# Kernel tuning notes

Measured on AMD Instinct MI355X. Metric: run time of the kernel, lower is better.

## Reference

```python
import jax, jax.numpy as jnp
import numpy as np

RADIUS = 0.1
NSAMPLE = 32
STRIDE = 4
EPS = 1e-5


def fps(p, M):
    # Furthest point sampling. p: [B, N, 3] -> idx [B, M] int32. First point is index 0.
    B, N, _ = p.shape

    def body(carry, _):
        dmin, last = carry
        lp = jnp.take_along_axis(p, last[:, None, None], axis=1)  # [B,1,3]
        d = jnp.sum((p - lp) ** 2, axis=-1)                       # [B,N]
        dmin = jnp.minimum(dmin, d)
        nxt = jnp.argmax(dmin, axis=-1).astype(jnp.int32)
        return (dmin, nxt), nxt

    first = jnp.zeros((B,), jnp.int32)
    dmin0 = jnp.full((B, N), jnp.inf, p.dtype)
    _, rest = jax.lax.scan(body, (dmin0, first), None, length=M - 1)
    return jnp.concatenate([first[None, :], rest], axis=0).T  # [B,M]


def ball_query(new_p, p, radius, K):
    # For each query, first K support indices with dist < radius (CUDA ballquery semantics:
    # pad with first found index; 0 if none). new_p [B,M,3], p [B,N,3] -> [B,M,K] int32.
    N = p.shape[1]
    d2 = (jnp.sum(new_p ** 2, -1)[:, :, None] + jnp.sum(p ** 2, -1)[:, None, :]
          - 2.0 * jnp.einsum('bmd,bnd->bmn', new_p, p))  # [B,M,N]
    scores = jnp.where(d2 < radius * radius,
                       jnp.arange(N, dtype=jnp.int32)[None, None, :], N)
    neg_vals, _ = jax.lax.top_k(-scores, K)  # K smallest scores, ascending
    idx = -neg_vals
    first = jnp.where(idx[..., :1] >= N, 0, idx[..., :1])
    return jnp.where(idx >= N, first, idx)


def bn(x, g, b):
    # BatchNorm (training-mode batch stats) over all dims except channel dim 1.
    axes = tuple(i for i in range(x.ndim) if i != 1)
    m = jnp.mean(x, axes, keepdims=True)
    v = jnp.var(x, axes, keepdims=True)
    shape = (1, -1) + (1,) * (x.ndim - 2)
    return g.reshape(shape) * (x - m) * jax.lax.rsqrt(v + EPS) + b.reshape(shape)


def setup_inputs() -> dict:
    key = jax.random.key(0)
    ks = jax.random.split(key, 6)
    B, N, C = 4, 8192, 64
    return {
        'p': jax.random.uniform(ks[0], (B, N, 3), jnp.float32),
        'f': jax.random.normal(ks[1], (B, C, N), jnp.float32),
        'w1': jax.random.normal(ks[2], (64, 3 + C), jnp.float32) * 0.05,
        'g1': jnp.ones((64,), jnp.float32),
        'b1': jnp.zeros((64,), jnp.float32),
        'w2': jax.random.normal(ks[3], (128, 64), jnp.float32) * 0.05,
        'g2': jnp.ones((128,), jnp.float32),
        'b2': jnp.zeros((128,), jnp.float32),
        'w_skip': jax.random.normal(ks[4], (128, C), jnp.float32) * 0.05,
        'b_skip': jnp.zeros((128,), jnp.float32),
    }


def reference(p, f, w1, g1, b1, w2, g2, b2, w_skip, b_skip):
    B, N, _ = p.shape
    C = f.shape[1]
    M = N // STRIDE
    idx = fps(p, M)                                                # [B,M]
    new_p = jnp.take_along_axis(p, idx[:, :, None], axis=1)        # [B,M,3]
    # residual branch: gather sampled features, 1x1 conv1d skip
    fi = jnp.take_along_axis(f, jnp.broadcast_to(idx[:, None, :], (B, C, M)), axis=2)
    identity = jnp.einsum('oc,bcm->bom', w_skip, fi) + b_skip[None, :, None]
    # ball-query grouping
    nidx = ball_query(new_p, p, RADIUS, NSAMPLE)                   # [B,M,K]
    flat = nidx.reshape(B, 1, M * NSAMPLE)
    pj = jnp.take_along_axis(p.transpose(0, 2, 1),
                             jnp.broadcast_to(flat, (B, 3, M * NSAMPLE)),
                             axis=2).reshape(B, 3, M, NSAMPLE)
    dp = pj - new_p.transpose(0, 2, 1)[:, :, :, None]              # [B,3,M,K]
    fj = jnp.take_along_axis(f, jnp.broadcast_to(flat, (B, C, M * NSAMPLE)),
                             axis=2).reshape(B, C, M, NSAMPLE)
    x = jnp.concatenate([dp, fj], axis=1)                          # [B,3+C,M,K]
    # conv-bn-relu, conv-bn (last block no act because use_res)
    x = jax.nn.relu(bn(jnp.einsum('oc,bcmk->bomk', w1, x), g1, b1))
    x = bn(jnp.einsum('oc,bcmk->bomk', w2, x), g2, b2)
    fout = jnp.max(x, axis=-1)                                     # [B,128,M]
    fout = jax.nn.relu(fout + identity)
    return new_p, fout, idx
```

## Files before the change

### kernel.cpp

```cpp
#include <hip/hip_runtime.h>
#include <math.h>

#define BB 4
#define NP 8192
#define CF 64
#define MQ 2048
#define KS 32

#define WS_FT     0u
#define WS_NIDX   2097152u
#define WS_IDXI   2359296u
#define WS_ST1    2367488u
#define WS_ST2    2375680u
#define WS_SC1    2392064u
#define WS_SC2    2392192u
#define WS_MAXY2  2392448u
#define WS_W1P    3441024u

typedef float v2f __attribute__((ext_vector_type(2)));

__global__ __launch_bounds__(256) void transpose_f_kernel(
    const float* __restrict__ f, float* __restrict__ ft) {
  __shared__ float tile[64][65];
  int b = blockIdx.y;
  int n0 = blockIdx.x * 64;
  int cc = threadIdx.x >> 6;
  int nn = threadIdx.x & 63;
  #pragma unroll
  for (int r = 0; r < 16; ++r) {
    int c = cc * 16 + r;
    tile[c][nn] = f[((size_t)b * 64 + c) * NP + n0 + nn];
  }
  __syncthreads();
  #pragma unroll
  for (int r = 0; r < 16; ++r) {
    int nl = cc * 16 + r;
    ft[((size_t)b * NP + n0 + nl) * 64 + nn] = tile[nn][nl];
  }
}

__global__ void prep_w1_kernel(const float* __restrict__ w1, float* __restrict__ w1p) {
  int i = blockIdx.x * 256 + threadIdx.x;
  if (i < 64 * 68) {
    int o = i / 68, c = i % 68;
    w1p[i] = (c < 67) ? w1[o * 67 + c] : 0.0f;
  }
}

#define FPS_T 256
#define PPT 32

template <int CTRL>
__device__ __forceinline__ unsigned long long dpp_max_step(unsigned long long k) {
  int lo = (int)(unsigned)k;
  int hi = (int)(unsigned)(k >> 32);
  int slo = __builtin_amdgcn_update_dpp(0, lo, CTRL, 0xF, 0xF, true);
  int shi = __builtin_amdgcn_update_dpp(0, hi, CTRL, 0xF, 0xF, true);
  unsigned long long s =
      ((unsigned long long)(unsigned)shi << 32) | (unsigned long long)(unsigned)slo;
  return s > k ? s : k;
}

__global__ __launch_bounds__(256, 1) void fps_kernel(
    const float* __restrict__ p, float* __restrict__ out, int* __restrict__ idx_i) {
#pragma clang fp contract(off)
  __shared__ float4 sp4[NP];
  __shared__ int win[MQ];
  __shared__ unsigned long long cnd[3];
  int b = blockIdx.x;
  const float* pb = p + (size_t)b * NP * 3;
  float* out_newp = out;
  float* out_idxf = out + BB*MQ*3 + (size_t)BB*128*MQ;
  int t = threadIdx.x;

  v2f px2[16], py2[16], pz2[16], dmin2[16];
  #pragma unroll
  for (int k = 0; k < 16; ++k) {
    int i0 = (2*k) * FPS_T + t;
    int i1 = i0 + FPS_T;
    float x0 = pb[i0*3+0], y0 = pb[i0*3+1], z0 = pb[i0*3+2];
    float x1 = pb[i1*3+0], y1 = pb[i1*3+1], z1 = pb[i1*3+2];
    px2[k] = (v2f){x0, x1}; py2[k] = (v2f){y0, y1}; pz2[k] = (v2f){z0, z1};
    sp4[i0] = make_float4(x0, y0, z0, 0.0f);
    sp4[i1] = make_float4(x1, y1, z1, 0.0f);
    dmin2[k] = (v2f){INFINITY, INFINITY};
  }
  if (t < 3) cnd[t] = 0ull;
  if (t == 0) win[0] = 0;
  __syncthreads();
  float lx = sp4[0].x, ly = sp4[0].y, lz = sp4[0].z;
  unsigned nt = ~(unsigned)t;

  for (int j = 1; j < MQ; ++j) {
#pragma clang fp contract(off)
    v2f l2x = (v2f){lx, lx}, l2y = (v2f){ly, ly}, l2z = (v2f){lz, lz};
    float bv0 = -1.0f, bv1 = -1.0f;
    unsigned bn0 = 0u, bn1 = 0u;
    #pragma unroll
    for (int k = 0; k < 16; ++k) {
      v2f dx = px2[k] - l2x;
      v2f dy = py2[k] - l2y;
      v2f dz = pz2[k] - l2z;
      v2f dd = ((dx*dx) + (dy*dy)) + (dz*dz);
      v2f dm = __builtin_elementwise_min(dmin2[k], dd);
      dmin2[k] = dm;
      float m0 = dm.x, m1 = dm.y;
      bool g0 = m0 > bv0;
      bv0 = g0 ? m0 : bv0;
      bn0 = g0 ? (nt - (unsigned)((2*k) * FPS_T)) : bn0;
      bool g1 = m1 > bv1;
      bv1 = g1 ? m1 : bv1;
      bn1 = g1 ? (nt - (unsigned)((2*k+1) * FPS_T)) : bn1;
    }
    unsigned long long k0 =
        ((unsigned long long)__float_as_uint(bv0) << 32) | (unsigned long long)bn0;
    unsigned long long k1 =
        ((unsigned long long)__float_as_uint(bv1) << 32) | (unsigned long long)bn1;
    unsigned long long key = k0 > k1 ? k0 : k1;
    key = dpp_max_step<0x111>(key);
    key = dpp_max_step<0x112>(key);
    key = dpp_max_step<0x114>(key);
    key = dpp_max_step<0x118>(key);
    key = dpp_max_step<0x142>(key);
    key = dpp_max_step<0x143>(key);
    int slot = j % 3;
    if ((t & 63) == 63) atomicMax(&cnd[slot], key);
    __syncthreads();
    unsigned long long kw = cnd[slot];
    if (t == 0) cnd[(j + 2) % 3] = 0ull;
    int wi = (int)(~(unsigned)kw);
    float4 c = sp4[wi];
    lx = c.x; ly = c.y; lz = c.z;
    if (t == 0) win[j] = wi;
  }

  __syncthreads();
  #pragma unroll
  for (int k = 0; k < MQ / FPS_T; ++k) {
    int j = k * FPS_T + t;
    int wi = win[j];
    out_idxf[b*MQ + j] = (float)wi;
    idx_i[b*MQ + j] = wi;
    float4 c = sp4[wi];
    float* np_ = &out_newp[(size_t)(b*MQ + j) * 3];
    np_[0] = c.x; np_[1] = c.y; np_[2] = c.z;
  }
}

__global__ __launch_bounds__(256) void ballq_kernel(
    const float* __restrict__ p, const float* __restrict__ newp,
    int* __restrict__ nidx) {
  int qid = blockIdx.x * 4 + (threadIdx.x >> 6);
  int lane = threadIdx.x & 63;
  int b = qid >> 11;
  const float* pb = p + (size_t)b * NP * 3;
  float qx = newp[qid*3], qy = newp[qid*3+1], qz = newp[qid*3+2];
  float sq_q = __fadd_rn(__fadd_rn(__fmul_rn(qx,qx), __fmul_rn(qy,qy)), __fmul_rn(qz,qz));
  const float R2 = (float)(0.1 * 0.1);
  int found = 0, first = -1;
  int* outp = nidx + (size_t)qid * KS;
  for (int base = 0; base < NP; base += 64) {
    int n = base + lane;
    float x = pb[n*3], y = pb[n*3+1], z = pb[n*3+2];
    float sq_p = __fadd_rn(__fadd_rn(__fmul_rn(x,x), __fmul_rn(y,y)), __fmul_rn(z,z));
    float dot  = __fadd_rn(__fadd_rn(__fmul_rn(qx,x), __fmul_rn(qy,y)), __fmul_rn(qz,z));
    float d2   = __fadd_rn(__fadd_rn(sq_q, sq_p), __fmul_rn(-2.0f, dot));
    bool hit = d2 < R2;
    unsigned long long mask = __ballot(hit);
    if (mask) {
      if (first < 0) first = base + __builtin_ctzll(mask);
      int cnt = __popcll(mask);
      if (found < KS) {
        int rank = __popcll(mask & ((1ull << lane) - 1ull));
        if (hit && found + rank < KS) outp[found + rank] = n;
      }
      found += cnt;
      if (found >= KS) break;
    }
  }
  int fcl = found < KS ? found : KS;
  int padv = first < 0 ? 0 : first;
  if (lane >= fcl && lane < KS) outp[lane] = padv;
}

__global__ __launch_bounds__(256) void p1_kernel(
    const float* __restrict__ p, const float* __restrict__ newp,
    const float* __restrict__ ft, const int* __restrict__ nidx,
    const float* __restrict__ w1p, float* __restrict__ stats1) {
  __shared__ __align__(16) float xbuf[4][KS][68];
  __shared__ float wbs[4][64], wbq[4][64];
  int wv = threadIdx.x >> 6, lane = threadIdx.x & 63;
  int qid = blockIdx.x * 4 + wv;
  int b = qid >> 11;
  int nv = (lane < KS) ? nidx[(size_t)qid * KS + lane] : 0;
  float qx = newp[qid*3], qy = newp[qid*3+1], qz = newp[qid*3+2];
  for (int kk = 0; kk < KS; ++kk) {
    int n = __shfl(nv, kk);
    const float* fr = ft + ((size_t)b * NP + n) * 64;
    xbuf[wv][kk][3 + lane] = fr[lane];
    if (lane < 3) {
      const float* pp = p + ((size_t)b * NP + n) * 3;
      float qc = (lane == 0) ? qx : ((lane == 1) ? qy : qz);
      xbuf[wv][kk][lane] = __fsub_rn(pp[lane], qc);
    }
    if (lane == 3) xbuf[wv][kk][67] = 0.0f;
  }
  __syncthreads();
  const float4* wr = (const float4*)(w1p + lane * 68);
  float4 wreg[17];
  #pragma unroll
  for (int c4 = 0; c4 < 17; ++c4) wreg[c4] = wr[c4];
  float ss = 0.f, qq = 0.f;
  for (int kk = 0; kk < KS; ++kk) {
    const float4* xr = (const float4*)(&xbuf[wv][kk][0]);
    float acc = 0.f;
    #pragma unroll
    for (int c4 = 0; c4 < 17; ++c4) {
      float4 w = wreg[c4]; float4 x = xr[c4];
      acc += w.x*x.x + w.y*x.y + w.z*x.z + w.w*x.w;
    }
    ss += acc; qq += acc * acc;
  }
  wbs[wv][lane] = ss; wbq[wv][lane] = qq;
  __syncthreads();
  if (threadIdx.x < 64) {
    float s  = wbs[0][threadIdx.x] + wbs[1][threadIdx.x] + wbs[2][threadIdx.x] + wbs[3][threadIdx.x];
    float s2 = wbq[0][threadIdx.x] + wbq[1][threadIdx.x] + wbq[2][threadIdx.x] + wbq[3][threadIdx.x];
    int slice = blockIdx.x & 63;
    atomicAdd(&stats1[(slice*2+0)*64 + threadIdx.x], s);
    atomicAdd(&stats1[(slice*2+1)*64 + threadIdx.x], s2);
  }
}

__global__ void fin1_kernel(const float* __restrict__ stats1,
                            const float* __restrict__ g, const float* __restrict__ bb,
                            float* __restrict__ sc) {
  int o = threadIdx.x;
  float s = 0.f, q = 0.f;
  for (int sl = 0; sl < 64; ++sl) { s += stats1[(sl*2+0)*64+o]; q += stats1[(sl*2+1)*64+o]; }
  const float cnt = (float)(BB * MQ * KS);
  float mean = s / cnt;
  float var = q / cnt - mean * mean;
  float rstd = 1.0f / sqrtf(var + 1e-5f);
  float gs = g[o] * rstd;
  sc[o] = gs;
  sc[64+o] = bb[o] - mean * gs;
}

__global__ void fin2_kernel(const float* __restrict__ stats2,
                            const float* __restrict__ g, const float* __restrict__ bb,
                            float* __restrict__ sc) {
  int o = threadIdx.x;
  float s = 0.f, q = 0.f;
  for (int sl = 0; sl < 64; ++sl) { s += stats2[(sl*2+0)*128+o]; q += stats2[(sl*2+1)*128+o]; }
  const float cnt = (float)(BB * MQ * KS);
  float mean = s / cnt;
  float var = q / cnt - mean * mean;
  float rstd = 1.0f / sqrtf(var + 1e-5f);
  float gs = g[o] * rstd;
  sc[o] = gs;
  sc[128+o] = bb[o] - mean * gs;
}

__global__ __launch_bounds__(256) void p2_kernel(
    const float* __restrict__ p, const float* __restrict__ newp,
    const float* __restrict__ ft, const int* __restrict__ nidx,
    const float* __restrict__ w1p, const float* __restrict__ w2,
    const float* __restrict__ sc1,
    float* __restrict__ stats2, float* __restrict__ maxy2) {
  __shared__ __align__(16) float xbuf[4][KS][68];
  __shared__ float wbs[4][128], wbq[4][128];
  int wv = threadIdx.x >> 6, lane = threadIdx.x & 63;
  int qid = blockIdx.x * 4 + wv;
  int b = qid >> 11;
  int nv = (lane < KS) ? nidx[(size_t)qid * KS + lane] : 0;
  float qx = newp[qid*3], qy = newp[qid*3+1], qz = newp[qid*3+2];
  for (int kk = 0; kk < KS; ++kk) {
    int n = __shfl(nv, kk);
    const float* fr = ft + ((size_t)b * NP + n) * 64;
    xbuf[wv][kk][3 + lane] = fr[lane];
    if (lane < 3) {
      const float* pp = p + ((size_t)b * NP + n) * 3;
      float qc = (lane == 0) ? qx : ((lane == 1) ? qy : qz);
      xbuf[wv][kk][lane] = __fsub_rn(pp[lane], qc);
    }
    if (lane == 3) xbuf[wv][kk][67] = 0.0f;
  }
  __syncthreads();
  {
    const float4* wr = (const float4*)(w1p + lane * 68);
    float4 wreg[17];
    #pragma unroll
    for (int c4 = 0; c4 < 17; ++c4) wreg[c4] = wr[c4];
    float s1v = sc1[lane], t1v = sc1[64 + lane];
    for (int kk = 0; kk < KS; ++kk) {
      const float4* xr = (const float4*)(&xbuf[wv][kk][0]);
      float acc = 0.f;
      #pragma unroll
      for (int c4 = 0; c4 < 17; ++c4) {
        float4 w = wreg[c4]; float4 x = xr[c4];
        acc += w.x*x.x + w.y*x.y + w.z*x.z + w.w*x.w;
      }
      float h = fmaxf(0.0f, fmaf(acc, s1v, t1v));
      xbuf[wv][kk][lane] = h;
    }
  }
  const float4* w2a = (const float4*)(w2 + (size_t)lane * 64);
  const float4* w2b = (const float4*)(w2 + (size_t)(lane + 64) * 64);
  float4 wra[16], wrb[16];
  #pragma unroll
  for (int c4 = 0; c4 < 16; ++c4) { wra[c4] = w2a[c4]; wrb[c4] = w2b[c4]; }
  float ss0 = 0.f, qq0 = 0.f, mx0 = -INFINITY;
  float ss1 = 0.f, qq1 = 0.f, mx1 = -INFINITY;
  for (int kk = 0; kk < KS; ++kk) {
    const float4* hr = (const float4*)(&xbuf[wv][kk][0]);
    float a0 = 0.f, a1 = 0.f;
    #pragma unroll
    for (int c4 = 0; c4 < 16; ++c4) {
      float4 h4 = hr[c4];
      float4 wa = wra[c4]; float4 wb = wrb[c4];
      a0 += wa.x*h4.x + wa.y*h4.y + wa.z*h4.z + wa.w*h4.w;
      a1 += wb.x*h4.x + wb.y*h4.y + wb.z*h4.z + wb.w*h4.w;
    }
    ss0 += a0; qq0 += a0*a0; mx0 = fmaxf(mx0, a0);
    ss1 += a1; qq1 += a1*a1; mx1 = fmaxf(mx1, a1);
  }
  maxy2[(size_t)qid * 128 + lane] = mx0;
  maxy2[(size_t)qid * 128 + 64 + lane] = mx1;
  wbs[wv][lane] = ss0; wbs[wv][64+lane] = ss1;
  wbq[wv][lane] = qq0; wbq[wv][64+lane] = qq1;
  __syncthreads();
  if (threadIdx.x < 128) {
    float s  = wbs[0][threadIdx.x] + wbs[1][threadIdx.x] + wbs[2][threadIdx.x] + wbs[3][threadIdx.x];
    float s2 = wbq[0][threadIdx.x] + wbq[1][threadIdx.x] + wbq[2][threadIdx.x] + wbq[3][threadIdx.x];
    int slice = blockIdx.x & 63;
    atomicAdd(&stats2[(slice*2+0)*128 + threadIdx.x], s);
    atomicAdd(&stats2[(slice*2+1)*128 + threadIdx.x], s2);
  }
}

__global__ __launch_bounds__(256) void p3_kernel(
    const float* __restrict__ ft, const int* __restrict__ idx_i,
    const float* __restrict__ w_skip, const float* __restrict__ b_skip,
    const float* __restrict__ sc2, const float* __restrict__ maxy2,
    float* __restrict__ outf) {
  int wv = threadIdx.x >> 6, lane = threadIdx.x & 63;
  int qid = blockIdx.x * 4 + wv;
  int b = qid >> 11, m = qid & (MQ - 1);
  int n = idx_i[qid];
  const float4* f4 = (const float4*)(ft + ((size_t)b * NP + n) * 64);
  const float4* wa = (const float4*)(w_skip + (size_t)lane * 64);
  const float4* wb = (const float4*)(w_skip + (size_t)(lane + 64) * 64);
  float a0 = b_skip[lane], a1 = b_skip[lane + 64];
  #pragma unroll
  for (int c4 = 0; c4 < 16; ++c4) {
    float4 x = f4[c4]; float4 u = wa[c4]; float4 v = wb[c4];
    a0 += u.x*x.x + u.y*x.y + u.z*x.z + u.w*x.w;
    a1 += v.x*x.x + v.y*x.y + v.z*x.z + v.w*x.w;
  }
  float v0 = maxy2[(size_t)qid * 128 + lane];
  float v1 = maxy2[(size_t)qid * 128 + 64 + lane];
  float r0 = fmaxf(0.0f, fmaf(v0, sc2[lane],      sc2[128 + lane])      + a0);
  float r1 = fmaxf(0.0f, fmaf(v1, sc2[lane + 64], sc2[128 + lane + 64]) + a1);
  outf[((size_t)b * 128 + lane) * MQ + m] = r0;
  outf[((size_t)b * 128 + lane + 64) * MQ + m] = r1;
}

extern "C" void kernel_launch(void* const* d_in, const int* in_sizes, int n_in,
                              void* d_out, int out_size, void* d_ws, size_t ws_size,
                              hipStream_t stream) {
  (void)in_sizes; (void)n_in; (void)out_size; (void)ws_size;
  const float* p   = (const float*)d_in[0];
  const float* f   = (const float*)d_in[1];
  const float* w1  = (const float*)d_in[2];
  const float* g1  = (const float*)d_in[3];
  const float* b1  = (const float*)d_in[4];
  const float* w2  = (const float*)d_in[5];
  const float* g2  = (const float*)d_in[6];
  const float* b2  = (const float*)d_in[7];
  const float* wsk = (const float*)d_in[8];
  const float* bsk = (const float*)d_in[9];
  float* out = (float*)d_out;
  float* wsf = (float*)d_ws;

  float* ft    = wsf + WS_FT;
  int*   nidx  = (int*)(wsf + WS_NIDX);
  int*   idxi  = (int*)(wsf + WS_IDXI);
  float* st1   = wsf + WS_ST1;
  float* st2   = wsf + WS_ST2;
  float* sc1   = wsf + WS_SC1;
  float* sc2   = wsf + WS_SC2;
  float* maxy2 = wsf + WS_MAXY2;
  float* w1p   = wsf + WS_W1P;

  float* out_newp = out;
  float* out_f    = out + BB*MQ*3;

  (void)hipMemsetAsync(st1, 0, (8192 + 16384) * sizeof(float), stream);

  transpose_f_kernel<<<dim3(NP/64, BB), 256, 0, stream>>>(f, ft);
  prep_w1_kernel<<<17, 256, 0, stream>>>(w1, w1p);
  fps_kernel<<<BB, FPS_T, 0, stream>>>(p, out, idxi);
  ballq_kernel<<<BB*MQ/4, 256, 0, stream>>>(p, out_newp, nidx);
  p1_kernel<<<BB*MQ/4, 256, 0, stream>>>(p, out_newp, ft, nidx, w1p, st1);
  fin1_kernel<<<1, 64, 0, stream>>>(st1, g1, b1, sc1);
  p2_kernel<<<BB*MQ/4, 256, 0, stream>>>(p, out_newp, ft, nidx, w1p, w2, sc1, st2, maxy2);
  fin2_kernel<<<1, 128, 0, stream>>>(st2, g2, b2, sc2);
  p3_kernel<<<BB*MQ/4, 256, 0, stream>>>(ft, idxi, wsk, bsk, sc2, maxy2, out_f);
}
```

Before: 2.158 ms.

## Spatially sort points in FPS and skip threads whose bounding box cannot improve

The FPS kernel now buckets points into a 512-cell Morton grid via a shared-memory histogram, prefix scan and ballot-based scatter, so each thread owns 16 spatially adjacent points with a bounding box. Each iteration computes a lower bound on distance from the last selected point to the box. If that bound cannot lower the thread's cached maximum min-distance, the distance update is skipped and the cached key is reused. Block size doubles to 512 threads with 16 points each. This adds a costly sort prologue, and the 0.999 margin on the pruning test with a cached key must keep exact argmax tie semantics.

Measured after the change: 2.209 ms. 2.3% more time.

```diff
diff --git a/kernel.cpp b/kernel.cpp
--- a/kernel.cpp
+++ b/kernel.cpp
@@ -18,6 +18,7 @@
 #define WS_W1P    3441024u
 
 typedef float v2f __attribute__((ext_vector_type(2)));
+typedef unsigned long long u64;
 
 __global__ __launch_bounds__(256) void transpose_f_kernel(
     const float* __restrict__ f, float* __restrict__ ft) {
@@ -47,76 +48,151 @@
   }
 }
 
-#define FPS_T 256
-#define PPT 32
+#define FPS_T 512
+#define SLOTS 16
 
 template <int CTRL>
-__device__ __forceinline__ unsigned long long dpp_max_step(unsigned long long k) {
+__device__ __forceinline__ u64 dpp_max_step(u64 k) {
   int lo = (int)(unsigned)k;
   int hi = (int)(unsigned)(k >> 32);
   int slo = __builtin_amdgcn_update_dpp(0, lo, CTRL, 0xF, 0xF, true);
   int shi = __builtin_amdgcn_update_dpp(0, hi, CTRL, 0xF, 0xF, true);
-  unsigned long long s =
-      ((unsigned long long)(unsigned)shi << 32) | (unsigned long long)(unsigned)slo;
+  u64 s = ((u64)(unsigned)shi << 32) | (u64)(unsigned)slo;
   return s > k ? s : k;
 }
 
-__global__ __launch_bounds__(256, 1) void fps_kernel(
+__global__ __launch_bounds__(512, 1) void fps_kernel(
     const float* __restrict__ p, float* __restrict__ out, int* __restrict__ idx_i) {
 #pragma clang fp contract(off)
   __shared__ float4 sp4[NP];
   __shared__ int win[MQ];
-  __shared__ unsigned long long cnd[3];
+  __shared__ u64 cnd[3];
   int b = blockIdx.x;
   const float* pb = p + (size_t)b * NP * 3;
   float* out_newp = out;
   float* out_idxf = out + BB*MQ*3 + (size_t)BB*128*MQ;
   int t = threadIdx.x;
-
-  v2f px2[16], py2[16], pz2[16], dmin2[16];
-  #pragma unroll
-  for (int k = 0; k < 16; ++k) {
-    int i0 = (2*k) * FPS_T + t;
-    int i1 = i0 + FPS_T;
-    float x0 = pb[i0*3+0], y0 = pb[i0*3+1], z0 = pb[i0*3+2];
-    float x1 = pb[i1*3+0], y1 = pb[i1*3+1], z1 = pb[i1*3+2];
-    px2[k] = (v2f){x0, x1}; py2[k] = (v2f){y0, y1}; pz2[k] = (v2f){z0, z1};
-    sp4[i0] = make_float4(x0, y0, z0, 0.0f);
-    sp4[i1] = make_float4(x1, y1, z1, 0.0f);
-    dmin2[k] = (v2f){INFINITY, INFINITY};
+  int lane = t & 63;
+  int wv = t >> 6;
+
+  float tx[SLOTS], ty[SLOTS], tz[SLOTS];
+  int cells[SLOTS];
+  win[t] = 0;
+  __syncthreads();
+  #pragma unroll
+  for (int s = 0; s < SLOTS; ++s) {
+    int i = s * FPS_T + t;
+    float x = pb[i*3+0], y = pb[i*3+1], z = pb[i*3+2];
+    tx[s] = x; ty[s] = y; tz[s] = z;
+    int cx = (int)(x * 8.0f); cx = cx < 0 ? 0 : (cx > 7 ? 7 : cx);
+    int cy = (int)(y * 8.0f); cy = cy < 0 ? 0 : (cy > 7 ? 7 : cy);
+    int cz = (int)(z * 8.0f); cz = cz < 0 ? 0 : (cz > 7 ? 7 : cz);
+    int mx = (cx & 1) | ((cx & 2) << 2) | ((cx & 4) << 4);
+    int my = (cy & 1) | ((cy & 2) << 2) | ((cy & 4) << 4);
+    int mz = (cz & 1) | ((cz & 2) << 2) | ((cz & 4) << 4);
+    int cell = mx | (my << 1) | (mz << 2);
+    cells[s] = cell;
+    atomicAdd(&win[cell], 1);
+  }
+  __syncthreads();
+  {
+    int myCnt = win[t];
+    int* sA = win; int* sB = win + 512;
+    __syncthreads();
+    bool a2b = true;
+    for (int off = 1; off < 512; off <<= 1) {
+      int* src = a2b ? sA : sB; int* dst = a2b ? sB : sA;
+      int v = src[t];
+      if (t >= off) v += src[t - off];
+      dst[t] = v;
+      a2b = !a2b;
+      __syncthreads();
+    }
+    int incl = sB[t];
+    __syncthreads();
+    win[t] = incl - myCnt;
+  }
+  __syncthreads();
+  for (int w = 0; w < 8; ++w) {
+    if (wv == w) {
+      #pragma unroll
+      for (int s = 0; s < SLOTS; ++s) {
+        int c = cells[s];
+        u64 eq = ~0ull;
+        #pragma unroll
+        for (int bit = 0; bit < 9; ++bit) {
+          u64 bset = __ballot(((c >> bit) & 1) != 0);
+          eq &= (((c >> bit) & 1) ? bset : ~bset);
+        }
+        int rank = (int)__popcll(eq & ((1ull << lane) - 1ull));
+        int leader = (int)__builtin_ctzll(eq);
+        int base = 0;
+        if (lane == leader) base = atomicAdd(&win[c], (int)__popcll(eq));
+        base = __shfl(base, leader);
+        sp4[base + rank] = make_float4(tx[s], ty[s], tz[s],
+                                       __int_as_float(s * FPS_T + t));
+      }
+    }
+    __syncthreads();
+  }
+  unsigned notI[SLOTS];
+  float bminx = INFINITY, bminy = INFINITY, bminz = INFINITY;
+  float bmaxx = -INFINITY, bmaxy = -INFINITY, bmaxz = -INFINITY;
+  #pragma unroll
+  for (int s = 0; s < SLOTS; ++s) {
+    float4 q = sp4[t * SLOTS + s];
+    tx[s] = q.x; ty[s] = q.y; tz[s] = q.z;
+    notI[s] = ~(unsigned)__float_as_int(q.w);
+    bminx = fminf(bminx, q.x); bmaxx = fmaxf(bmaxx, q.x);
+    bminy = fminf(bminy, q.y); bmaxy = fmaxf(bmaxy, q.y);
+    bminz = fminf(bminz, q.z); bmaxz = fmaxf(bmaxz, q.z);
+  }
+  __syncthreads();
+  #pragma unroll
+  for (int s = 0; s < SLOTS; ++s) {
+    int oi = (int)(~notI[s]);
+    sp4[oi] = make_float4(tx[s], ty[s], tz[s], 0.0f);
   }
   if (t < 3) cnd[t] = 0ull;
   if (t == 0) win[0] = 0;
+  v2f px2[8], py2[8], pz2[8], dmin2[8];
+  #pragma unroll
+  for (int k = 0; k < 8; ++k) {
+    px2[k] = (v2f){tx[2*k], tx[2*k+1]};
+    py2[k] = (v2f){ty[2*k], ty[2*k+1]};
+    pz2[k] = (v2f){tz[2*k], tz[2*k+1]};
+    dmin2[k] = (v2f){INFINITY, INFINITY};
+  }
   __syncthreads();
   float lx = sp4[0].x, ly = sp4[0].y, lz = sp4[0].z;
-  unsigned nt = ~(unsigned)t;
-
+
+  float bvCache = INFINITY;
+  u64 cachedKey = 0ull;
   for (int j = 1; j < MQ; ++j) {
-#pragma clang fp contract(off)
-    v2f l2x = (v2f){lx, lx}, l2y = (v2f){ly, ly}, l2z = (v2f){lz, lz};
-    float bv0 = -1.0f, bv1 = -1.0f;
-    unsigned bn0 = 0u, bn1 = 0u;
-    #pragma unroll
-    for (int k = 0; k < 16; ++k) {
-      v2f dx = px2[k] - l2x;
-      v2f dy = py2[k] - l2y;
-      v2f dz = pz2[k] - l2z;
-      v2f dd = ((dx*dx) + (dy*dy)) + (dz*dz);
-      v2f dm = __builtin_elementwise_min(dmin2[k], dd);
-      dmin2[k] = dm;
-      float m0 = dm.x, m1 = dm.y;
-      bool g0 = m0 > bv0;
-      bv0 = g0 ? m0 : bv0;
-      bn0 = g0 ? (nt - (unsigned)((2*k) * FPS_T)) : bn0;
-      bool g1 = m1 > bv1;
-      bv1 = g1 ? m1 : bv1;
-      bn1 = g1 ? (nt - (unsigned)((2*k+1) * FPS_T)) : bn1;
-    }
-    unsigned long long k0 =
-        ((unsigned long long)__float_as_uint(bv0) << 32) | (unsigned long long)bn0;
-    unsigned long long k1 =
-        ((unsigned long long)__float_as_uint(bv1) << 32) | (unsigned long long)bn1;
-    unsigned long long key = k0 > k1 ? k0 : k1;
+    float dxm = fmaxf(fmaxf(bminx - lx, lx - bmaxx), 0.0f);
+    float dym = fmaxf(fmaxf(bminy - ly, ly - bmaxy), 0.0f);
+    float dzm = fmaxf(fmaxf(bminz - lz, lz - bmaxz), 0.0f);
+    float lbsq = dxm*dxm + dym*dym + dzm*dzm;
+    if (!(lbsq * 0.999f >= bvCache)) {
+      v2f l2x = (v2f){lx, lx}, l2y = (v2f){ly, ly}, l2z = (v2f){lz, lz};
+      u64 c0 = 0ull, c1 = 0ull;
+      #pragma unroll
+      for (int k = 0; k < 8; ++k) {
+        v2f dx = px2[k] - l2x;
+        v2f dy = py2[k] - l2y;
+        v2f dz = pz2[k] - l2z;
+        v2f dd = ((dx*dx) + (dy*dy)) + (dz*dz);
+        v2f dm = __builtin_elementwise_min(dmin2[k], dd);
+        dmin2[k] = dm;
+        u64 k0 = ((u64)__float_as_uint(dm.x) << 32) | (u64)notI[2*k];
+        u64 k1 = ((u64)__float_as_uint(dm.y) << 32) | (u64)notI[2*k+1];
+        c0 = k0 > c0 ? k0 : c0;
+        c1 = k1 > c1 ? k1 : c1;
+      }
+      cachedKey = c0 > c1 ? c0 : c1;
+      bvCache = __uint_as_float((unsigned)(cachedKey >> 32));
+    }
+    u64 key = cachedKey;
     key = dpp_max_step<0x111>(key);
     key = dpp_max_step<0x112>(key);
     key = dpp_max_step<0x114>(key);
@@ -124,9 +200,9 @@
     key = dpp_max_step<0x142>(key);
     key = dpp_max_step<0x143>(key);
     int slot = j % 3;
-    if ((t & 63) == 63) atomicMax(&cnd[slot], key);
+    if (lane == 63) atomicMax(&cnd[slot], key);
     __syncthreads();
-    unsigned long long kw = cnd[slot];
+    u64 kw = cnd[slot];
     if (t == 0) cnd[(j + 2) % 3] = 0ull;
     int wi = (int)(~(unsigned)kw);
     float4 c = sp4[wi];
@@ -136,8 +212,8 @@
 
   __syncthreads();
   #pragma unroll
-  for (int k = 0; k < MQ / FPS_T; ++k) {
-    int j = k * FPS_T + t;
+  for (int k2 = 0; k2 < MQ / FPS_T; ++k2) {
+    int j = k2 * FPS_T + t;
     int wi = win[j];
     out_idxf[b*MQ + j] = (float)wi;
     idx_i[b*MQ + j] = wi;
```
